# Kernel optimization log

Measured on AMD Instinct MI355X. Metric: run time of the kernel, lower is better.

Reference implementation:

```python
import jax, jax.numpy as jnp
import numpy as np

EPS = 1e-9
TOP_K = 2


def setup_inputs() -> dict:
    key = jax.random.key(0)
    k = jax.random.split(key, 6)
    B, E, D_IN, D_MODEL, D_SEL = 16384, 8, 900, 512, 128
    return {
        "cycle_curve_data": jax.random.normal(k[0], (B, D_IN), jnp.float32),
        "logits": jax.random.normal(k[1], (B, E), jnp.float32),
        "moe_masks": jax.random.randint(k[2], (B, E), 0, 2, jnp.int32),
        "selection_embeddings": jax.random.normal(k[3], (B, E, D_SEL), jnp.float32),
        "W": jax.random.normal(k[4], (E, D_IN, D_MODEL), jnp.float32) / np.sqrt(D_IN).astype(np.float32),
        "b": jnp.zeros((E, D_MODEL), jnp.float32),
    }


def reference(cycle_curve_data, logits, moe_masks, selection_embeddings, W, b):
    B, E = logits.shape
    mask = (moe_masks == 1).astype(logits.dtype)  # [B, E]
    raw = jax.nn.softmax(logits, axis=1)          # [B, E]

    # inactive-expert mixture for selection embedding
    inactive = raw * (1.0 - mask)
    inactive = inactive / (jnp.sum(inactive, axis=1, keepdims=True) + EPS)
    selection_embedding = jnp.einsum("bes,be->bs", selection_embeddings, inactive)

    # active gates + top-k selection + renormalization
    active = raw * mask
    _, idx = jax.lax.top_k(active, TOP_K)                                  # [B, K]
    top_mask = jnp.sum(jax.nn.one_hot(idx, E, dtype=active.dtype), axis=1)  # [B, E]
    gates = active * top_mask
    gates = gates / (jnp.sum(gates, axis=1, keepdims=True) + EPS)

    # dense formulation of dispatch -> per-expert Linear -> weighted combine:
    # out[b] = sum_e gates[b,e] * (x[b] @ W[e] + b[e])
    expert_out = jnp.einsum("bd,edm->bem", cycle_curve_data, W) + b  # [B, E, D_model]
    final_out = jnp.einsum("bem,be->bm", expert_out, gates).astype(jnp.bfloat16)

    # guide loss (training-mode auxiliary loss)
    s = jnp.sum(raw * mask) / B
    guide_loss = (1.0 - s) * (1.0 - s)
    return final_out, guide_loss, selection_embedding
```

## Files before the change

### kernel.cpp

```cpp
#include <hip/hip_runtime.h>
#include <hip/hip_bf16.h>


#define B_ROWS 16384
#define DIN 900
#define DM 512
#define DSEL 128
#define KP 928
#define NKS 29
#define MAXT 192
#define EPSF 1e-9f

#define OUT_GUIDE (B_ROWS*DM)
#define OUT_SEL   (B_ROWS*DM + 1)

#define WS_COUNTS 0
#define WS_PART   512
#define WS_NT     768
#define WS_OFF    1024
#define WS_ENT    2048
#define WS_BB     9216
#define WS_PIDLR  25600
#define WS_GATEB  91136
#define WS_W8     222208
#define WS_ROWSS  746496
#define WS_WT     812032

typedef __attribute__((ext_vector_type(8))) short short8;
typedef __attribute__((ext_vector_type(8))) unsigned short ushort8;
typedef __attribute__((ext_vector_type(4))) float floatx4;

__device__ inline unsigned short f2bf(float v){
  union { __hip_bfloat16 h; unsigned short u; } c;
  c.h = __float2bfloat16(v);
  return c.u;
}
__device__ inline float bf2f(unsigned short u){
  union { unsigned int i; float f; } c;
  c.i = ((unsigned int)u) << 16;
  return c.f;
}
__device__ inline ushort8 pack8u(float4 a, float4 b){
  ushort8 c;
  c[0]=f2bf(a.x); c[1]=f2bf(a.y); c[2]=f2bf(a.z); c[3]=f2bf(a.w);
  c[4]=f2bf(b.x); c[5]=f2bf(b.y); c[6]=f2bf(b.z); c[7]=f2bf(b.w);
  return c;
}

__global__ __launch_bounds__(256) void cvtw2_k(const float* __restrict__ W,
                                               unsigned short* __restrict__ wt2){
  __shared__ unsigned short lds[32][512];
  int t = threadIdx.x;
  int kc = blockIdx.x, e = blockIdx.y;
  for (int kk = 0; kk < 32; ++kk){
    int k = kc*32 + kk;
    if (k < DIN){
      const float* wr = W + ((size_t)e*DIN + k)*DM;
      lds[kk][t]       = f2bf(wr[t]);
      lds[kk][t + 256] = f2bf(wr[t + 256]);
    } else {
      lds[kk][t] = 0; lds[kk][t + 256] = 0;
    }
  }
  __syncthreads();
  int ncg = t >> 3, q = t & 7;
  unsigned short* ob = wt2 + (((size_t)e*32 + ncg)*29 + kc)*512;
  for (int i = 0; i < 8; ++i){
    int fb = i*64 + q*8;
    int col = fb >> 5, kk0 = fb & 31;
    ushort8 y;
    #pragma unroll
    for (int j = 0; j < 8; ++j) y[j] = lds[kk0 + j][ncg*16 + col];
    *((ushort8*)(ob + fb)) = y;
  }
}

__global__ __launch_bounds__(256) void gating_k(const float* __restrict__ logits,
                                                const int* __restrict__ masks,
                                                int* __restrict__ counts,
                                                float* __restrict__ partials,
                                                int* __restrict__ pidlr,
                                                float2* __restrict__ gatesb,
                                                float* __restrict__ w8,
                                                int* __restrict__ blockbase){
  __shared__ int hist[64];
  __shared__ float wsum[4];
  int t = threadIdx.x;
  if (t < 64) hist[t] = 0;
  __syncthreads();
  int b = blockIdx.x*256 + t;
  float4 l0 = *(const float4*)&logits[(size_t)b*8];
  float4 l1 = *(const float4*)&logits[(size_t)b*8 + 4];
  int4  m0 = *(const int4*)&masks[(size_t)b*8];
  int4  m1 = *(const int4*)&masks[(size_t)b*8 + 4];
  float raw[8] = {l0.x,l0.y,l0.z,l0.w,l1.x,l1.y,l1.z,l1.w};
  int   mk[8]  = {m0.x,m0.y,m0.z,m0.w,m1.x,m1.y,m1.z,m1.w};
  float mx = raw[0];
  for (int e = 1; e < 8; e++) mx = fmaxf(mx, raw[e]);
  float Z = 0.f;
  for (int e = 0; e < 8; e++){ raw[e] = expf(raw[e]-mx); Z += raw[e]; }
  float invZ = 1.f/Z;
  float act[8], ina[8]; float srm = 0.f, isum = 0.f;
  for (int e = 0; e < 8; e++){
    raw[e] *= invZ;
    if (mk[e] == 1){ act[e] = raw[e]; ina[e] = 0.f; srm += raw[e]; }
    else           { act[e] = 0.f;    ina[e] = raw[e]; isum += raw[e]; }
  }
  float v1 = -1.f, v2 = -1.f; int e1 = 0, e2 = 0;
  for (int e = 0; e < 8; e++){
    float a = act[e];
    if (a > v1){ v2 = v1; e2 = e1; v1 = a; e1 = e; }
    else if (a > v2){ v2 = a; e2 = e; }
  }
  float den = v1 + v2 + EPSF;
  float g1 = v1/den, g2 = v2/den;
  int lo, hi; float gl, gh;
  if (e1 < e2){ lo = e1; hi = e2; gl = g1; gh = g2; }
  else        { lo = e2; hi = e1; gl = g2; gh = g1; }
  int pid = lo*8 + hi;
  float invI = 1.f/(isum + EPSF);
  for (int e = 0; e < 8; e++) w8[(size_t)b*8 + e] = ina[e]*invI;
  gatesb[b] = make_float2(gl, gh);
  int lr = atomicAdd(&hist[pid], 1);
  pidlr[b] = pid | (lr << 8);
  float s = srm;
  for (int sft = 32; sft > 0; sft >>= 1) s += __shfl_down(s, sft, 64);
  if ((t & 63) == 0) wsum[t >> 6] = s;
  __syncthreads();
  if (t < 64){
    int c = hist[t];
    int base = 0;
    if (c > 0) base = atomicAdd(&counts[t], c);
    blockbase[blockIdx.x*64 + t] = base;
  }
  if (t == 0) partials[blockIdx.x] = wsum[0] + wsum[1] + wsum[2] + wsum[3];
}

__global__ __launch_bounds__(256) void selemb_k(const float* __restrict__ sel,
                                                const float* __restrict__ w8,
                                                const int* __restrict__ pidlr,
                                                const int* __restrict__ off,
                                                const int* __restrict__ blockbase,
                                                int* __restrict__ rows_s,
                                                float* __restrict__ out){
  int t = threadIdx.x;
  int b = blockIdx.x*2 + (t >> 7);
  int d = t & 127;
  if (d == 0){
    int pl = pidlr[b];
    int p = pl & 63;
    int lr = pl >> 8;
    rows_s[off[p] + blockbase[(b >> 8)*64 + p] + lr] = b;
  }
  const float* wr = w8 + (size_t)b*8;
  const float* sb = sel + (size_t)b*(8*DSEL);
  float a = 0.f;
  for (int e = 0; e < 8; e++) a += wr[e] * sb[e*DSEL + d];
  out[OUT_SEL + (size_t)b*DSEL + d] = a;
}

__global__ void worklist_k(const int* __restrict__ counts,
                           const float* __restrict__ partials,
                           int* __restrict__ off, int* __restrict__ ntp,
                           int4* __restrict__ entries,
                           float* __restrict__ out){
  int lane = threadIdx.x;
  int c = counts[lane];
  int sc = c;
  for (int s = 1; s < 64; s <<= 1){ int v = __shfl_up(sc, s, 64); if (lane >= s) sc += v; }
  int offp = sc - c;
  off[lane] = offp;
  int nt = (c + 127) >> 7;
  int snt = nt;
  for (int s = 1; s < 64; s <<= 1){ int v = __shfl_up(snt, s, 64); if (lane >= s) snt += v; }
  int tbase = snt - nt;
  int elo = lane >> 3, ehi = lane & 7;
  for (int j = 0; j < nt; ++j){
    int nr = c - j*128; if (nr > 128) nr = 128;
    entries[tbase + j] = make_int4(elo, ehi, offp + j*128, nr);
  }
  int tot = __shfl(snt, 63, 64);
  if (lane == 0) *ntp = tot;
  float p = partials[lane];
  for (int s = 32; s > 0; s >>= 1) p += __shfl_down(p, s, 64);
  if (lane == 0){
    float sv = p * (1.f/B_ROWS);
    float d = 1.f - sv;
    out[OUT_GUIDE] = d*d;
  }
}


#define ALOAD(kk) { \
  if ((kk) < 28){ \
    const float4* p = (const float4*)(xrow + (kk)*32); \
    a0 = p[0]; a1 = p[1]; a2 = p[2]; a3 = p[3]; \
  } else { \
    float tmp[16]; \
    _Pragma("unroll") \
    for (int j = 0; j < 16; ++j){ \
      int k = (kk)*32 + skc*16 + j; \
      tmp[j] = (k < DIN) ? xrow[(kk)*32 + j] : 0.f; \
    } \
    a0 = make_float4(tmp[0],tmp[1],tmp[2],tmp[3]); \
    a1 = make_float4(tmp[4],tmp[5],tmp[6],tmp[7]); \
    a2 = make_float4(tmp[8],tmp[9],tmp[10],tmp[11]); \
    a3 = make_float4(tmp[12],tmp[13],tmp[14],tmp[15]); \
  } }

#define BLOAD(kk) { \
  bw0 = *((const ushort8*)(bg0 + (size_t)(kk)*512)); \
  bw1 = *((const ushort8*)(bg1 + (size_t)(kk)*512)); \
  bw2 = *((const ushort8*)(bg2 + (size_t)(kk)*512)); \
  bw3 = *((const ushort8*)(bg3 + (size_t)(kk)*512)); }

#define AWRITE(buf) { \
  *((ushort8*)&as_[buf][srow*40 + skc*16])     = pack8u(a0, a1); \
  *((ushort8*)&as_[buf][srow*40 + skc*16 + 8]) = pack8u(a2, a3); }

#define BWRITE(buf) { \
  *((ushort8*)&bs_[buf][bl0]) = bw0; \
  *((ushort8*)&bs_[buf][bl1]) = bw1; \
  *((ushort8*)&bs_[buf][bl2]) = bw2; \
  *((ushort8*)&bs_[buf][bl3]) = bw3; }

__global__ __launch_bounds__(256, 2) void gemm_k(const float* __restrict__ xf,
                                                 const unsigned short* __restrict__ wt2,
                                                 const float* __restrict__ bias,
                                                 const int* __restrict__ ntp,
                                                 const int4* __restrict__ entries,
                                                 const int* __restrict__ rows_s,
                                                 const float2* __restrict__ gatesb,
                                                 float* __restrict__ out){
  int tile = blockIdx.x;
  if (tile >= *ntp) return;
  int4 ent = entries[tile];
  int elo = ent.x, ehi = ent.y, start = ent.z, nrows = ent.w;

  __shared__ __align__(16) unsigned short as_[2][128*40];
  __shared__ __align__(16) unsigned short bs_[2][16*16*40];
  __shared__ int   gidx_s[128];
  __shared__ float glo_s[128];
  __shared__ float ghi_s[128];

  int t = threadIdx.x;
  if (t < 128){
    if (t < nrows){
      int g = rows_s[start + t];
      gidx_s[t] = g;
      float2 gg = gatesb[g];
      glo_s[t] = gg.x; ghi_s[t] = gg.y;
    } else { gidx_s[t] = -1; glo_s[t] = 0.f; ghi_s[t] = 0.f; }
  }
  __syncthreads();

  int lane = t & 63, wid = t >> 6;
  int wrow = wid >> 1, wcol = wid & 1;
  int quad = lane >> 4, l16 = lane & 15;

  int srow = t >> 1, skc = t & 1;
  int sg = gidx_s[srow];
  const float* xrow = xf + (size_t)(sg >= 0 ? sg : 0)*DIN + skc*16;

  int bcol = (t & 63) >> 2, bq = t & 3;
  const unsigned short* bg0; const unsigned short* bg1;
  const unsigned short* bg2; const unsigned short* bg3;
  int bl0, bl1, bl2, bl3;
  {
    int u0 = t, u1 = 256 + t, u2 = 512 + t, u3 = 768 + t;
    int j0 = (u0 >> 6) & 7, j1 = (u1 >> 6) & 7, j2 = (u2 >> 6) & 7, j3 = (u3 >> 6) & 7;
    int goff = (t & 63)*8;
    bg0 = wt2 + ((size_t)(elo*32 + blockIdx.y*8 + j0)*29)*512 + goff;
    bg1 = wt2 + ((size_t)(elo*32 + blockIdx.y*8 + j1)*29)*512 + goff;
    bg2 = wt2 + ((size_t)(ehi*32 + blockIdx.y*8 + j2)*29)*512 + goff;
    bg3 = wt2 + ((size_t)(ehi*32 + blockIdx.y*8 + j3)*29)*512 + goff;
    bl0 = ((0*8 + j0)*16 + bcol)*40 + bq*8;
    bl1 = ((0*8 + j1)*16 + bcol)*40 + bq*8;
    bl2 = ((1*8 + j2)*16 + bcol)*40 + bq*8;
    bl3 = ((1*8 + j3)*16 + bcol)*40 + bq*8;
  }

  floatx4 acc[2][4][4];
  #pragma unroll
  for (int i = 0; i < 2; i++)
    #pragma unroll
    for (int j = 0; j < 4; j++)
      #pragma unroll
      for (int k = 0; k < 4; k++)
        #pragma unroll
        for (int r = 0; r < 4; r++) acc[i][j][k][r] = 0.f;

  float4 a0, a1, a2, a3;
  ushort8 bw0, bw1, bw2, bw3;

  ALOAD(0); BLOAD(0);
  AWRITE(0); BWRITE(0);
  __syncthreads();

  for (int ks = 0; ks < NKS; ++ks){
    int cur = ks & 1;
    int nk = ks + 1;
    if (nk < NKS){ ALOAD(nk); BLOAD(nk); }

    short8 af[4];
    #pragma unroll
    for (int mt = 0; mt < 4; ++mt)
      af[mt] = *((const short8*)&as_[cur][(wrow*64 + mt*16 + l16)*40 + quad*8]);
    #pragma unroll
    for (int e = 0; e < 2; ++e){
      #pragma unroll
      for (int nt = 0; nt < 4; ++nt){
        short8 bfr = *((const short8*)&bs_[cur][((e*8 + wcol*4 + nt)*16 + l16)*40 + quad*8]);
        #pragma unroll
        for (int mt = 0; mt < 4; ++mt)
          acc[e][mt][nt] = __builtin_amdgcn_mfma_f32_16x16x32_bf16(af[mt], bfr, acc[e][mt][nt], 0, 0, 0);
      }
    }

    if (nk < NKS){ AWRITE(cur ^ 1); BWRITE(cur ^ 1); }
    __syncthreads();
  }

  int colbase = blockIdx.y*128 + wcol*64;
  float blo[4], bhi[4];
  #pragma unroll
  for (int nt = 0; nt < 4; ++nt){
    int n = colbase + nt*16 + l16;
    blo[nt] = bias[elo*DM + n];
    bhi[nt] = bias[ehi*DM + n];
  }
  #pragma unroll
  for (int mt = 0; mt < 4; ++mt){
    #pragma unroll
    for (int r = 0; r < 4; ++r){
      int rr = wrow*64 + mt*16 + quad*4 + r;
      int grow = gidx_s[rr];
      if (grow >= 0){
        float2 gg = gatesb[grow];
        float* orow = out + (size_t)grow*DM;
        #pragma unroll
        for (int nt = 0; nt < 4; ++nt){
          int n = colbase + nt*16 + l16;
          float v = gg.x*(acc[0][mt][nt][r] + blo[nt]) + gg.y*(acc[1][mt][nt][r] + bhi[nt]);
          orow[n] = bf2f(f2bf(v));
        }
      }
    }
  }
}

extern "C" void kernel_launch(void* const* d_in, const int* in_sizes, int n_in,
                              void* d_out, int out_size, void* d_ws, size_t ws_size,
                              hipStream_t stream){
  const float* x      = (const float*)d_in[0];
  const float* logits = (const float*)d_in[1];
  const int*   masks  = (const int*)d_in[2];
  const float* sel    = (const float*)d_in[3];
  const float* W      = (const float*)d_in[4];
  const float* bias   = (const float*)d_in[5];
  float* out = (float*)d_out;
  char* ws = (char*)d_ws;
  int*    counts   = (int*)(ws + WS_COUNTS);
  float*  partials = (float*)(ws + WS_PART);
  int*    ntp      = (int*)(ws + WS_NT);
  int*    off      = (int*)(ws + WS_OFF);
  int4*   entries  = (int4*)(ws + WS_ENT);
  int*    blockbase= (int*)(ws + WS_BB);
  int*    pidlr    = (int*)(ws + WS_PIDLR);
  float2* gatesb   = (float2*)(ws + WS_GATEB);
  float*  w8       = (float*)(ws + WS_W8);
  int*    rows_s   = (int*)(ws + WS_ROWSS);
  unsigned short* wt2 = (unsigned short*)(ws + WS_WT);

  hipMemsetAsync(ws, 0, 256, stream);
  cvtw2_k<<<dim3(29, 8), 256, 0, stream>>>(W, wt2);
  gating_k<<<B_ROWS/256, 256, 0, stream>>>(logits, masks, counts, partials, pidlr, gatesb, w8, blockbase);
  worklist_k<<<1, 64, 0, stream>>>(counts, partials, off, ntp, entries, out);
  selemb_k<<<B_ROWS/2, 256, 0, stream>>>(sel, w8, pidlr, off, blockbase, rows_s, out);
  gemm_k<<<dim3(MAXT, 4), 256, 0, stream>>>(x, wt2, bias, ntp, entries, rows_s, gatesb, out);
}
```

Measured before the change: 286.2 us.

## Load expert weight fragments straight into registers and remap tiles for L2 reuse

The GEMM no longer stages expert weights through shared memory. Each wave loads its bf16 B fragments directly from global memory into registers, prefetching one fragment ahead of the MFMA groups. The A tile keeps double buffering, with the row stride shrunk to 36 and the k-loop manually unrolled into even/odd register sets. A 1-D grid with a swizzled tile/column mapping groups the four column blocks of neighbouring tiles so their weights are shared through cache. This cuts LDS traffic and footprint, at the cost of more global load latency per wave, more register pressure, and possible LDS bank conflicts from the 36-element stride.

```diff
diff --git a/kernel.cpp b/kernel.cpp
--- a/kernel.cpp
+++ b/kernel.cpp
@@ -25,6 +25,8 @@
 #define WS_W8     222208
 #define WS_ROWSS  746496
 #define WS_WT     812032
+
+#define FRSTRIDE 14848
 
 typedef __attribute__((ext_vector_type(8))) short short8;
 typedef __attribute__((ext_vector_type(8))) unsigned short ushort8;
@@ -191,38 +193,56 @@
 }
 
 
-#define ALOAD(kk) { \
-  if ((kk) < 28){ \
-    const float4* p = (const float4*)(xrow + (kk)*32); \
-    a0 = p[0]; a1 = p[1]; a2 = p[2]; a3 = p[3]; \
-  } else { \
-    float tmp[16]; \
-    _Pragma("unroll") \
-    for (int j = 0; j < 16; ++j){ \
-      int k = (kk)*32 + skc*16 + j; \
-      tmp[j] = (k < DIN) ? xrow[(kk)*32 + j] : 0.f; \
-    } \
-    a0 = make_float4(tmp[0],tmp[1],tmp[2],tmp[3]); \
-    a1 = make_float4(tmp[4],tmp[5],tmp[6],tmp[7]); \
-    a2 = make_float4(tmp[8],tmp[9],tmp[10],tmp[11]); \
-    a3 = make_float4(tmp[12],tmp[13],tmp[14],tmp[15]); \
-  } }
-
-#define BLOAD(kk) { \
-  bw0 = *((const ushort8*)(bg0 + (size_t)(kk)*512)); \
-  bw1 = *((const ushort8*)(bg1 + (size_t)(kk)*512)); \
-  bw2 = *((const ushort8*)(bg2 + (size_t)(kk)*512)); \
-  bw3 = *((const ushort8*)(bg3 + (size_t)(kk)*512)); }
-
-#define AWRITE(buf) { \
-  *((ushort8*)&as_[buf][srow*40 + skc*16])     = pack8u(a0, a1); \
-  *((ushort8*)&as_[buf][srow*40 + skc*16 + 8]) = pack8u(a2, a3); }
-
-#define BWRITE(buf) { \
-  *((ushort8*)&bs_[buf][bl0]) = bw0; \
-  *((ushort8*)&bs_[buf][bl1]) = bw1; \
-  *((ushort8*)&bs_[buf][bl2]) = bw2; \
-  *((ushort8*)&bs_[buf][bl3]) = bw3; }
+#define ALOADV(P, kk) { \
+  const float4* p_ = (const float4*)(xrow + (kk)*32); \
+  P##0 = p_[0]; P##1 = p_[1]; P##2 = p_[2]; P##3 = p_[3]; }
+
+#define ALOADT(P) { \
+  float tmp[16]; \
+  _Pragma("unroll") \
+  for (int j = 0; j < 16; ++j){ \
+    int k = 896 + skc*16 + j; \
+    tmp[j] = (k < DIN) ? xrow[28*32 + j] : 0.f; \
+  } \
+  P##0 = make_float4(tmp[0],tmp[1],tmp[2],tmp[3]); \
+  P##1 = make_float4(tmp[4],tmp[5],tmp[6],tmp[7]); \
+  P##2 = make_float4(tmp[8],tmp[9],tmp[10],tmp[11]); \
+  P##3 = make_float4(tmp[12],tmp[13],tmp[14],tmp[15]); }
+
+#define AWR(buf, P) { \
+  *((ushort8*)&as_[buf][srow*36 + skc*16])     = pack8u(P##0, P##1); \
+  *((ushort8*)&as_[buf][srow*36 + skc*16 + 8]) = pack8u(P##2, P##3); }
+
+#define MFJ(j) { \
+  acc[0][0][j] = __builtin_amdgcn_mfma_f32_16x16x32_bf16(af0, b0c, acc[0][0][j], 0, 0, 0); \
+  acc[0][1][j] = __builtin_amdgcn_mfma_f32_16x16x32_bf16(af1, b0c, acc[0][1][j], 0, 0, 0); \
+  acc[0][2][j] = __builtin_amdgcn_mfma_f32_16x16x32_bf16(af2, b0c, acc[0][2][j], 0, 0, 0); \
+  acc[0][3][j] = __builtin_amdgcn_mfma_f32_16x16x32_bf16(af3, b0c, acc[0][3][j], 0, 0, 0); \
+  acc[1][0][j] = __builtin_amdgcn_mfma_f32_16x16x32_bf16(af0, b1c, acc[1][0][j], 0, 0, 0); \
+  acc[1][1][j] = __builtin_amdgcn_mfma_f32_16x16x32_bf16(af1, b1c, acc[1][1][j], 0, 0, 0); \
+  acc[1][2][j] = __builtin_amdgcn_mfma_f32_16x16x32_bf16(af2, b1c, acc[1][2][j], 0, 0, 0); \
+  acc[1][3][j] = __builtin_amdgcn_mfma_f32_16x16x32_bf16(af3, b1c, acc[1][3][j], 0, 0, 0); }
+
+#define KSTEP(ks, cur, LAST) { \
+  short8 af0 = *((const short8*)&as_[cur][(wrow*64 +  0 + l16)*36 + quad*8]); \
+  short8 af1 = *((const short8*)&as_[cur][(wrow*64 + 16 + l16)*36 + quad*8]); \
+  short8 af2 = *((const short8*)&as_[cur][(wrow*64 + 32 + l16)*36 + quad*8]); \
+  short8 af3 = *((const short8*)&as_[cur][(wrow*64 + 48 + l16)*36 + quad*8]); \
+  short8 b0n, b1n; \
+  b0n = *((const short8*)(bp0 + 1*FRSTRIDE + (size_t)(ks)*512)); \
+  b1n = *((const short8*)(bp1 + 1*FRSTRIDE + (size_t)(ks)*512)); \
+  MFJ(0); b0c = b0n; b1c = b1n; \
+  b0n = *((const short8*)(bp0 + 2*FRSTRIDE + (size_t)(ks)*512)); \
+  b1n = *((const short8*)(bp1 + 2*FRSTRIDE + (size_t)(ks)*512)); \
+  MFJ(1); b0c = b0n; b1c = b1n; \
+  b0n = *((const short8*)(bp0 + 3*FRSTRIDE + (size_t)(ks)*512)); \
+  b1n = *((const short8*)(bp1 + 3*FRSTRIDE + (size_t)(ks)*512)); \
+  MFJ(2); b0c = b0n; b1c = b1n; \
+  if (!(LAST)){ \
+    b0n = *((const short8*)(bp0 + (size_t)((ks)+1)*512)); \
+    b1n = *((const short8*)(bp1 + (size_t)((ks)+1)*512)); \
+  } \
+  MFJ(3); b0c = b0n; b1c = b1n; }
 
 __global__ __launch_bounds__(256, 2) void gemm_k(const float* __restrict__ xf,
                                                  const unsigned short* __restrict__ wt2,
@@ -232,13 +252,14 @@
                                                  const int* __restrict__ rows_s,
                                                  const float2* __restrict__ gatesb,
                                                  float* __restrict__ out){
-  int tile = blockIdx.x;
+  int id = blockIdx.x;
+  int tile = (id >> 5)*8 + (id & 7);
+  int y = (id >> 3) & 3;
   if (tile >= *ntp) return;
   int4 ent = entries[tile];
   int elo = ent.x, ehi = ent.y, start = ent.z, nrows = ent.w;
 
-  __shared__ __align__(16) unsigned short as_[2][128*40];
-  __shared__ __align__(16) unsigned short bs_[2][16*16*40];
+  __shared__ __align__(16) unsigned short as_[2][128*36];
   __shared__ int   gidx_s[128];
   __shared__ float glo_s[128];
   __shared__ float ghi_s[128];
@@ -257,28 +278,14 @@
   int lane = t & 63, wid = t >> 6;
   int wrow = wid >> 1, wcol = wid & 1;
   int quad = lane >> 4, l16 = lane & 15;
+  int ncg0 = y*8 + wcol*4;
 
   int srow = t >> 1, skc = t & 1;
   int sg = gidx_s[srow];
   const float* xrow = xf + (size_t)(sg >= 0 ? sg : 0)*DIN + skc*16;
 
-  int bcol = (t & 63) >> 2, bq = t & 3;
-  const unsigned short* bg0; const unsigned short* bg1;
-  const unsigned short* bg2; const unsigned short* bg3;
-  int bl0, bl1, bl2, bl3;
-  {
-    int u0 = t, u1 = 256 + t, u2 = 512 + t, u3 = 768 + t;
-    int j0 = (u0 >> 6) & 7, j1 = (u1 >> 6) & 7, j2 = (u2 >> 6) & 7, j3 = (u3 >> 6) & 7;
-    int goff = (t & 63)*8;
-    bg0 = wt2 + ((size_t)(elo*32 + blockIdx.y*8 + j0)*29)*512 + goff;
-    bg1 = wt2 + ((size_t)(elo*32 + blockIdx.y*8 + j1)*29)*512 + goff;
-    bg2 = wt2 + ((size_t)(ehi*32 + blockIdx.y*8 + j2)*29)*512 + goff;
-    bg3 = wt2 + ((size_t)(ehi*32 + blockIdx.y*8 + j3)*29)*512 + goff;
-    bl0 = ((0*8 + j0)*16 + bcol)*40 + bq*8;
-    bl1 = ((0*8 + j1)*16 + bcol)*40 + bq*8;
-    bl2 = ((1*8 + j2)*16 + bcol)*40 + bq*8;
-    bl3 = ((1*8 + j3)*16 + bcol)*40 + bq*8;
-  }
+  const unsigned short* bp0 = wt2 + ((size_t)(elo*32 + ncg0))*FRSTRIDE + l16*32 + quad*8;
+  const unsigned short* bp1 = wt2 + ((size_t)(ehi*32 + ncg0))*FRSTRIDE + l16*32 + quad*8;
 
   floatx4 acc[2][4][4];
   #pragma unroll
@@ -290,38 +297,29 @@
         #pragma unroll
         for (int r = 0; r < 4; r++) acc[i][j][k][r] = 0.f;
 
-  float4 a0, a1, a2, a3;
-  ushort8 bw0, bw1, bw2, bw3;
-
-  ALOAD(0); BLOAD(0);
-  AWRITE(0); BWRITE(0);
-  __syncthreads();
-
-  for (int ks = 0; ks < NKS; ++ks){
-    int cur = ks & 1;
-    int nk = ks + 1;
-    if (nk < NKS){ ALOAD(nk); BLOAD(nk); }
-
-    short8 af[4];
-    #pragma unroll
-    for (int mt = 0; mt < 4; ++mt)
-      af[mt] = *((const short8*)&as_[cur][(wrow*64 + mt*16 + l16)*40 + quad*8]);
-    #pragma unroll
-    for (int e = 0; e < 2; ++e){
-      #pragma unroll
-      for (int nt = 0; nt < 4; ++nt){
-        short8 bfr = *((const short8*)&bs_[cur][((e*8 + wcol*4 + nt)*16 + l16)*40 + quad*8]);
-        #pragma unroll
-        for (int mt = 0; mt < 4; ++mt)
-          acc[e][mt][nt] = __builtin_amdgcn_mfma_f32_16x16x32_bf16(af[mt], bfr, acc[e][mt][nt], 0, 0, 0);
-      }
-    }
-
-    if (nk < NKS){ AWRITE(cur ^ 1); BWRITE(cur ^ 1); }
+  float4 rE0, rE1, rE2, rE3;
+  float4 rO0, rO1, rO2, rO3;
+
+  ALOADV(rE, 0);
+  ALOADV(rO, 1);
+  AWR(0, rE);
+  short8 b0c = *((const short8*)(bp0));
+  short8 b1c = *((const short8*)(bp1));
+  __syncthreads();
+
+  for (int ks = 0; ks < 28; ks += 2){
+    if (ks < 26){ ALOADV(rE, ks+2); } else { ALOADT(rE); }
+    KSTEP(ks, 0, false);
+    AWR(1, rO);
     __syncthreads();
-  }
-
-  int colbase = blockIdx.y*128 + wcol*64;
+    if (ks < 26){ ALOADV(rO, ks+3); }
+    KSTEP(ks+1, 1, false);
+    AWR(0, rE);
+    __syncthreads();
+  }
+  KSTEP(28, 0, true);
+
+  int colbase = y*128 + wcol*64;
   float blo[4], bhi[4];
   #pragma unroll
   for (int nt = 0; nt < 4; ++nt){
@@ -377,5 +375,5 @@
   gating_k<<<B_ROWS/256, 256, 0, stream>>>(logits, masks, counts, partials, pidlr, gatesb, w8, blockbase);
   worklist_k<<<1, 64, 0, stream>>>(counts, partials, off, ntp, entries, out);
   selemb_k<<<B_ROWS/2, 256, 0, stream>>>(sel, w8, pidlr, off, blockbase, rows_s, out);
-  gemm_k<<<dim3(MAXT, 4), 256, 0, stream>>>(x, wt2, bias, ntp, entries, rows_s, gatesb, out);
-}
+  gemm_k<<<4*MAXT, 256, 0, stream>>>(x, wt2, bias, ntp, entries, rows_s, gatesb, out);
+}
```

After: 324.8 us. 13.5% more time.
